# Kernel optimization log

Measured on AMD Instinct MI355X. Metric: run time of the kernel, lower is better.

The kernel has to match this reference:

```python
import jax, jax.numpy as jnp
import numpy as np

NUM_HEADS = 8
NEG_INF = float(-2**32 + 1)
LN_EPS = 1e-8


def setup_inputs() -> dict:
    key = jax.random.key(0)
    ks = jax.random.split(key, 9)
    B, T, D = 4, 2048, 512
    inp = {
        "queries": jax.random.normal(ks[0], (B, T, D), jnp.float32),
        "keys": jax.random.normal(ks[1], (B, T, D), jnp.float32),
        "values": jax.random.normal(ks[2], (B, T, D), jnp.float32),
        "Wq": jax.random.normal(ks[3], (D, D), jnp.float32) / np.sqrt(D),
        "bq": jnp.zeros((D,), jnp.float32),
        "Wk": jax.random.normal(ks[4], (D, D), jnp.float32) / np.sqrt(D),
        "bk": jnp.zeros((D,), jnp.float32),
        "Wv": jax.random.normal(ks[5], (D, D), jnp.float32) / np.sqrt(D),
        "bv": jnp.zeros((D,), jnp.float32),
        "gamma": jnp.ones((D,), jnp.float32),
        "beta": jnp.zeros((D,), jnp.float32),
    }
    return inp


def _split_heads(x, h):
    # torch.cat(torch.chunk(x, h, dim=2), dim=0): [B,T,D] -> [h*B, T, D/h], head-major
    B, T, D = x.shape
    return x.reshape(B, T, h, D // h).transpose(2, 0, 1, 3).reshape(h * B, T, D // h)


def _merge_heads(x, h, B):
    # inverse: [h*B, T, dh] -> [B, T, h*dh]
    hB, T, dh = x.shape
    return x.reshape(h, B, T, dh).transpose(1, 2, 0, 3).reshape(B, T, h * dh)


def reference(queries, keys, values, Wq, bq, Wk, bk, Wv, bv, gamma, beta):
    h = NUM_HEADS
    B, Tq, D = queries.shape
    dh = D // h

    Q = jax.nn.relu(queries @ Wq + bq)
    K = jax.nn.relu(keys @ Wk + bk)
    V = jax.nn.relu(values @ Wv + bv)

    Q_ = _split_heads(Q, h)  # [h*B, Tq, dh]
    K_ = _split_heads(K, h)
    V_ = _split_heads(V, h)

    scores = jnp.einsum('bqd,bkd->bqk', Q_, K_) / jnp.sqrt(jnp.float32(dh))  # [h*B, Tq, Tk]

    # key padding mask: zero rows in `keys` get -inf scores
    key_mask = jnp.sign(jnp.abs(jnp.sum(keys, axis=-1)))  # [B, Tk]
    key_mask = jnp.tile(key_mask, (h, 1))  # [h*B, Tk]
    scores = jnp.where(key_mask[:, None, :] == 0.0, NEG_INF, scores)

    attn = jax.nn.softmax(scores, axis=-1)

    # query mask applied multiplicatively post-softmax
    query_mask = jnp.sign(jnp.abs(jnp.sum(queries, axis=-1)))  # [B, Tq]
    query_mask = jnp.tile(query_mask, (h, 1))  # [h*B, Tq]
    attn = attn * query_mask[:, :, None]

    out = jnp.einsum('bqk,bkd->bqd', attn, V_)  # [h*B, Tq, dh]
    out = _merge_heads(out, h, B) + queries  # residual

    # custom LayerNorm: torch.std is unbiased (ddof=1), eps added to std
    mean = out.mean(-1, keepdims=True)
    std = jnp.sqrt(out.var(-1, ddof=1, keepdims=True))
    return gamma * (out - mean) / (std + LN_EPS) + beta
```

## Files before the change

### kernel.cpp

```cpp
#include <hip/hip_runtime.h>


typedef __attribute__((ext_vector_type(8))) __bf16 bf16x8;
typedef __attribute__((ext_vector_type(4))) float f32x4;

#if __has_builtin(__builtin_amdgcn_exp2f)
#define EXP2F __builtin_amdgcn_exp2f
#else
#define EXP2F exp2f
#endif

#define QSCALE (0.125f * 1.4426950408889634f)

__device__ __forceinline__ unsigned short f2bf(float f) {
  return __builtin_bit_cast(unsigned short, (__bf16)f);
}
__device__ __forceinline__ unsigned pk2(float a, float b) {
  return (unsigned)f2bf(a) | ((unsigned)f2bf(b) << 16);
}
__device__ __forceinline__ f32x4 mfma16(bf16x8 a, bf16x8 b, f32x4 c) {
  return __builtin_amdgcn_mfma_f32_16x16x32_bf16(a, b, c, 0, 0, 0);
}
__device__ __forceinline__ bf16x8 ld_bf8(const unsigned short* p) {
  return *(const bf16x8*)p;
}
__device__ __forceinline__ void g2l16(const void* g, void* l) {
  __builtin_amdgcn_global_load_lds(
      (const __attribute__((address_space(1))) void*)g,
      (__attribute__((address_space(3))) void*)l, 16, 0, 0);
}

__global__ __launch_bounds__(256) void wt_kernel(const float* __restrict__ Wq,
                                                 const float* __restrict__ Wk,
                                                 const float* __restrict__ Wv,
                                                 unsigned short* __restrict__ Wt) {
  int idx = blockIdx.x * 256 + threadIdx.x;
  int o = idx * 8;
  int z = o >> 18;
  int rem = o & 262143;
  int n = rem >> 9;
  int k0 = rem & 511;
  const float* W = (z == 0) ? Wq : ((z == 1) ? Wk : Wv);
  unsigned int w[4];
#pragma unroll
  for (int i = 0; i < 4; ++i) {
    unsigned short lo = f2bf(W[(k0 + 2 * i) * 512 + n]);
    unsigned short hi = f2bf(W[(k0 + 2 * i + 1) * 512 + n]);
    w[i] = (unsigned)lo | ((unsigned)hi << 16);
  }
  *(uint4*)(Wt + o) = make_uint4(w[0], w[1], w[2], w[3]);
}

__global__ __launch_bounds__(256) void mask_kernel(const float* __restrict__ q,
                                                   const float* __restrict__ k,
                                                   float* __restrict__ qmask,
                                                   float* __restrict__ kmask) {
  int w = blockIdx.x * 4 + (threadIdx.x >> 6);
  int lane = threadIdx.x & 63;
  const float* src = (w < 8192) ? q : k;
  int row = w & 8191;
  const float4* p = (const float4*)(src + row * 512);
  float4 v1 = p[lane];
  float4 v2 = p[64 + lane];
  float s = v1.x + v1.y + v1.z + v1.w + v2.x + v2.y + v2.z + v2.w;
#pragma unroll
  for (int off = 32; off > 0; off >>= 1) s += __shfl_xor(s, off);
  if (lane == 0) {
    float m = (s == 0.0f) ? 0.0f : 1.0f;
    if (w < 8192) qmask[row] = m; else kmask[row] = m;
  }
}

__global__ __launch_bounds__(256, 3) void proj_kernel(
    const float* __restrict__ Xq, const float* __restrict__ Xk,
    const float* __restrict__ Xv, const float* __restrict__ bq,
    const float* __restrict__ bk, const float* __restrict__ bv,
    const unsigned short* __restrict__ Wt, unsigned short* __restrict__ Qb,
    unsigned short* __restrict__ Kb, unsigned short* __restrict__ Vt) {
  __shared__ float Asm[2][128][16];
  __shared__ unsigned short Bsm[128][32];

  int tid = threadIdx.x;
  int m0g = blockIdx.x * 128;
  int z = m0g >> 13;
  int m0 = m0g & 8191;
  int n0 = blockIdx.y * 128;
  const float* X = (z == 0) ? Xq : ((z == 1) ? Xk : Xv);
  const float* bias = (z == 0) ? bq : ((z == 1) ? bk : bv);
  const unsigned short* Wz = Wt + z * 262144;

  int w = tid >> 6, lane = tid & 63;
  int wm = w >> 1, wn = w & 1;
  int mrow = lane & 15, quad = lane >> 4;

  int srow = tid >> 2, schk = tid & 3;
  const float* gA = X + (m0 + srow) * 512 + schk * 4;
  const unsigned short* gB = Wz + (n0 + srow) * 512 + schk * 8;
  char* lA = (char*)&Asm[0][0][0] + tid * 16;
  char* lB = (char*)&Bsm[0][0] + tid * 16;

  const float* rA = &Asm[quad >> 1][0][(quad & 1) * 8];
  const unsigned short* rB = &Bsm[0][quad * 8];

  f32x4 zero = {0.f, 0.f, 0.f, 0.f};
  f32x4 acc[4][4];
#pragma unroll
  for (int i = 0; i < 4; ++i)
#pragma unroll
    for (int j = 0; j < 4; ++j) acc[i][j] = zero;

  for (int kc = 0; kc < 16; ++kc) {
    int ko = kc * 32;
    g2l16(gA + ko, lA);
    g2l16(gA + ko + 64 * 512, lA + 4096);
    g2l16(gA + ko + 16, lA + 8192);
    g2l16(gA + ko + 16 + 64 * 512, lA + 12288);
    g2l16(gB + ko, lB);
    g2l16(gB + ko + 64 * 512, lB + 4096);
    __syncthreads();

    bf16x8 af[4], bfr[4];
#pragma unroll
    for (int mt = 0; mt < 4; ++mt) {
      const float* pa = rA + (wm * 64 + mt * 16 + mrow) * 16;
      f32x4 lo = *(const f32x4*)pa;
      f32x4 hi = *(const f32x4*)(pa + 4);
      bf16x8 t;
      t[0] = (__bf16)lo[0]; t[1] = (__bf16)lo[1];
      t[2] = (__bf16)lo[2]; t[3] = (__bf16)lo[3];
      t[4] = (__bf16)hi[0]; t[5] = (__bf16)hi[1];
      t[6] = (__bf16)hi[2]; t[7] = (__bf16)hi[3];
      af[mt] = t;
    }
#pragma unroll
    for (int nt = 0; nt < 4; ++nt)
      bfr[nt] = ld_bf8(rB + (wn * 64 + nt * 16 + mrow) * 32);
#pragma unroll
    for (int mt = 0; mt < 4; ++mt)
#pragma unroll
      for (int nt = 0; nt < 4; ++nt)
        acc[mt][nt] = mfma16(af[mt], bfr[nt], acc[mt][nt]);
    __syncthreads();
  }

  if (z < 2) {
    unsigned short* dst = (z == 0) ? Qb : Kb;
    float sc = (z == 0) ? QSCALE : 1.0f;
#pragma unroll
    for (int nt = 0; nt < 4; ++nt) {
      int n = n0 + wn * 64 + nt * 16 + mrow;
      float bv_ = bias[n];
#pragma unroll
      for (int mt = 0; mt < 4; ++mt) {
        int m = m0 + wm * 64 + mt * 16 + quad * 4;
#pragma unroll
        for (int r = 0; r < 4; ++r) {
          float v = fmaxf(acc[mt][nt][r] + bv_, 0.f) * sc;
          dst[(m + r) * 512 + n] = f2bf(v);
        }
      }
    }
  } else {
#pragma unroll
    for (int nt = 0; nt < 4; ++nt) {
      int n = n0 + wn * 64 + nt * 16 + mrow;
      int hh = n >> 6, jj = n & 63;
      float bv_ = bias[n];
#pragma unroll
      for (int mt = 0; mt < 4; ++mt) {
        int grow = m0 + wm * 64 + mt * 16 + quad * 4;
        int bb = grow >> 11, tl = grow & 2047;
        float p0 = fmaxf(acc[mt][nt][0] + bv_, 0.f);
        float p1 = fmaxf(acc[mt][nt][1] + bv_, 0.f);
        float p2 = fmaxf(acc[mt][nt][2] + bv_, 0.f);
        float p3 = fmaxf(acc[mt][nt][3] + bv_, 0.f);
        *(uint2*)(Vt + ((hh * 4 + bb) * 64 + jj) * 2048 + tl) =
            make_uint2(pk2(p0, p1), pk2(p2, p3));
      }
    }
  }
}

__global__ __launch_bounds__(256) void attn_kernel(
    const unsigned short* __restrict__ Qb, const unsigned short* __restrict__ Kb,
    const unsigned short* __restrict__ Vt, const float* __restrict__ qmask,
    const float* __restrict__ kmask, const float* __restrict__ queries,
    float* __restrict__ out) {
  __shared__ unsigned short plds[4][64 * 40];
  __shared__ float lbuf[4][64];
  float* Obuf = (float*)&plds[0][0];

  int hb = blockIdx.x;
  int qt = blockIdx.y;
  int h = hb >> 2, b = hb & 3;
  int q0 = qt * 64;
  int tid = threadIdx.x;
  int w = tid >> 6, lane = tid & 63;
  int mrow = lane & 15, quad = lane >> 4;
  unsigned short* pw = &plds[w][0];

  bf16x8 qf[4][2];
  {
    const unsigned short* qp = Qb + (b * 2048 + q0 + mrow) * 512 + h * 64 + quad * 8;
#pragma unroll
    for (int qn = 0; qn < 4; ++qn) {
      qf[qn][0] = ld_bf8(qp + qn * 8192);
      qf[qn][1] = ld_bf8(qp + qn * 8192 + 32);
    }
  }

  f32x4 zero = {0.f, 0.f, 0.f, 0.f};
  f32x4 oacc[4][4];
#pragma unroll
  for (int i = 0; i < 4; ++i)
#pragma unroll
    for (int j = 0; j < 4; ++j) oacc[i][j] = zero;
  float lpart[4] = {0.f, 0.f, 0.f, 0.f};

  const int kidx = (b * 2048 + w * 32 + mrow) * 512 + h * 64 + quad * 8;
  const int vidx = (hb * 64 + mrow) * 2048 + w * 32 + quad * 8;
  const int kmi = b * 2048 + w * 32 + quad * 4;
  const int pbase = mrow * 40 + quad * 4;
  const int prd = mrow * 40 + quad * 8;

  bf16x8 kf[2][2];
#pragma unroll
  for (int mt = 0; mt < 2; ++mt) {
    kf[mt][0] = ld_bf8(Kb + kidx + mt * 8192);
    kf[mt][1] = ld_bf8(Kb + kidx + mt * 8192 + 32);
  }

  for (int it = 0; it < 16; ++it) {
    int kb = it << 7;
    f32x4 sacc[2][4];
#pragma unroll
    for (int mt = 0; mt < 2; ++mt)
#pragma unroll
      for (int qn = 0; qn < 4; ++qn) {
        f32x4 s = mfma16(kf[mt][0], qf[qn][0], zero);
        sacc[mt][qn] = mfma16(kf[mt][1], qf[qn][1], s);
      }
    bf16x8 vf[4];
#pragma unroll
    for (int dt = 0; dt < 4; ++dt) vf[dt] = ld_bf8(Vt + vidx + dt * 32768 + kb);
    f32x4 km[2];
    km[0] = *(const f32x4*)(kmask + kmi + kb);
    km[1] = *(const f32x4*)(kmask + kmi + kb + 16);
#pragma unroll
    for (int mt = 0; mt < 2; ++mt)
#pragma unroll
      for (int qn = 0; qn < 4; ++qn) {
        f32x4 p;
#pragma unroll
        for (int r = 0; r < 4; ++r) p[r] = EXP2F(sacc[mt][qn][r]) * km[mt][r];
        lpart[qn] += p[0] + p[1] + p[2] + p[3];
        *(uint2*)(pw + qn * 640 + pbase + mt * 16) =
            make_uint2(pk2(p[0], p[1]), pk2(p[2], p[3]));
      }
    bf16x8 pf[4];
#pragma unroll
    for (int qn = 0; qn < 4; ++qn) pf[qn] = ld_bf8(pw + qn * 640 + prd);
    int nkb = ((it + 1) & 15) << 7;
    bf16x8 nkf[2][2];
#pragma unroll
    for (int mt = 0; mt < 2; ++mt) {
      nkf[mt][0] = ld_bf8(Kb + kidx + nkb * 512 + mt * 8192);
      nkf[mt][1] = ld_bf8(Kb + kidx + nkb * 512 + mt * 8192 + 32);
    }
#pragma unroll
    for (int dt = 0; dt < 4; ++dt)
#pragma unroll
      for (int qn = 0; qn < 4; ++qn)
        oacc[dt][qn] = mfma16(vf[dt], pf[qn], oacc[dt][qn]);
#pragma unroll
    for (int mt = 0; mt < 2; ++mt) {
      kf[mt][0] = nkf[mt][0];
      kf[mt][1] = nkf[mt][1];
    }
  }

#pragma unroll
  for (int qn = 0; qn < 4; ++qn) {
    lpart[qn] += __shfl_xor(lpart[qn], 16);
    lpart[qn] += __shfl_xor(lpart[qn], 32);
  }
  if (quad == 0) {
#pragma unroll
    for (int qn = 0; qn < 4; ++qn) lbuf[w][qn * 16 + mrow] = lpart[qn];
  }
  __syncthreads();

  for (int ph = 0; ph < 4; ++ph) {
    if (w == ph) {
#pragma unroll
      for (int dt = 0; dt < 4; ++dt)
#pragma unroll
        for (int qn = 0; qn < 4; ++qn) {
          float* dst = Obuf + (qn * 16 + mrow) * 68 + dt * 16 + quad * 4;
          f32x4 v = oacc[dt][qn];
          if (ph) {
            v[0] += dst[0]; v[1] += dst[1]; v[2] += dst[2]; v[3] += dst[3];
          }
          dst[0] = v[0]; dst[1] = v[1]; dst[2] = v[2]; dst[3] = v[3];
        }
    }
    __syncthreads();
  }

#pragma unroll
  for (int i = 0; i < 4; ++i) {
    int qr = w * 16 + i * 4 + quad;
    float l = lbuf[0][qr] + lbuf[1][qr] + lbuf[2][qr] + lbuf[3][qr];
    int qg = b * 2048 + q0 + qr;
    float inv = qmask[qg] / l;
    const float* ob = Obuf + qr * 68 + mrow * 4;
    const float4 res = *(const float4*)(queries + qg * 512 + h * 64 + mrow * 4);
    float4 r;
    r.x = ob[0] * inv + res.x;
    r.y = ob[1] * inv + res.y;
    r.z = ob[2] * inv + res.z;
    r.w = ob[3] * inv + res.w;
    *(float4*)(out + qg * 512 + h * 64 + mrow * 4) = r;
  }
}

__global__ __launch_bounds__(256) void ln_kernel(float* __restrict__ out,
                                                 const float* __restrict__ gamma,
                                                 const float* __restrict__ beta) {
  int row = blockIdx.x * 4 + (threadIdx.x >> 6);
  int lane = threadIdx.x & 63;
  float* p = out + row * 512;
  float4 v1 = ((const float4*)p)[lane];
  float4 v2 = ((const float4*)p)[64 + lane];
  float s = v1.x + v1.y + v1.z + v1.w + v2.x + v2.y + v2.z + v2.w;
  float sq = v1.x * v1.x + v1.y * v1.y + v1.z * v1.z + v1.w * v1.w +
             v2.x * v2.x + v2.y * v2.y + v2.z * v2.z + v2.w * v2.w;
#pragma unroll
  for (int off = 32; off > 0; off >>= 1) {
    s += __shfl_xor(s, off);
    sq += __shfl_xor(sq, off);
  }
  float mean = s * (1.f / 512.f);
  float var = fmaxf((sq - 512.f * mean * mean) * (1.f / 511.f), 0.f);
  float inv = 1.f / (sqrtf(var) + 1e-8f);
  float4 g1 = ((const float4*)gamma)[lane];
  float4 g2 = ((const float4*)gamma)[64 + lane];
  float4 b1 = ((const float4*)beta)[lane];
  float4 b2 = ((const float4*)beta)[64 + lane];
  v1.x = g1.x * (v1.x - mean) * inv + b1.x;
  v1.y = g1.y * (v1.y - mean) * inv + b1.y;
  v1.z = g1.z * (v1.z - mean) * inv + b1.z;
  v1.w = g1.w * (v1.w - mean) * inv + b1.w;
  v2.x = g2.x * (v2.x - mean) * inv + b2.x;
  v2.y = g2.y * (v2.y - mean) * inv + b2.y;
  v2.z = g2.z * (v2.z - mean) * inv + b2.z;
  v2.w = g2.w * (v2.w - mean) * inv + b2.w;
  ((float4*)p)[lane] = v1;
  ((float4*)p)[64 + lane] = v2;
}

extern "C" void kernel_launch(void* const* d_in, const int* in_sizes, int n_in,
                              void* d_out, int out_size, void* d_ws, size_t ws_size,
                              hipStream_t stream) {
  (void)in_sizes; (void)n_in; (void)out_size; (void)ws_size;
  const float* queries = (const float*)d_in[0];
  const float* keys    = (const float*)d_in[1];
  const float* values  = (const float*)d_in[2];
  const float* Wq = (const float*)d_in[3];
  const float* bq = (const float*)d_in[4];
  const float* Wk = (const float*)d_in[5];
  const float* bk = (const float*)d_in[6];
  const float* Wv = (const float*)d_in[7];
  const float* bv = (const float*)d_in[8];
  const float* gamma = (const float*)d_in[9];
  const float* beta  = (const float*)d_in[10];
  float* out = (float*)d_out;

  char* ws = (char*)d_ws;
  unsigned short* Qb = (unsigned short*)(ws);
  unsigned short* Kb = (unsigned short*)(ws + 8 * 1024 * 1024);
  unsigned short* Vt = (unsigned short*)(ws + 16 * 1024 * 1024);
  unsigned short* Wt = (unsigned short*)(ws + 24 * 1024 * 1024);
  float* qmask = (float*)(ws + 24 * 1024 * 1024 + 3 * 512 * 512 * 2);
  float* kmask = qmask + 8192;

  wt_kernel<<<384, 256, 0, stream>>>(Wq, Wk, Wv, Wt);
  mask_kernel<<<4096, 256, 0, stream>>>(queries, keys, qmask, kmask);
  proj_kernel<<<dim3(192, 4), 256, 0, stream>>>(queries, keys, values, bq, bk, bv,
                                                Wt, Qb, Kb, Vt);
  attn_kernel<<<dim3(32, 32), 256, 0, stream>>>(Qb, Kb, Vt, qmask, kmask, queries, out);
  ln_kernel<<<2048, 256, 0, stream>>>(out, gamma, beta);
}
```

Before: 215.7 us.

## Feed softmax probabilities directly from registers into PV MFMA, drop LDS staging

Removes the per-wave LDS round-trip that converted the score accumulator layout into the B-operand layout for the P·V MFMA. Instead, the V operand is loaded with a permuted k-index (two 4-element chunks) so the probabilities packed straight from the S accumulators line up with it. The row-sum is now computed with an extra MFMA against a vector of ones instead of scalar adds and cross-lane shuffles. This cuts LDS traffic and shuffles but adds MFMA work and splits each V fragment into two narrower global loads.

```diff
diff --git a/kernel.cpp b/kernel.cpp
--- a/kernel.cpp
+++ b/kernel.cpp
@@ -186,9 +186,8 @@
     const unsigned short* __restrict__ Vt, const float* __restrict__ qmask,
     const float* __restrict__ kmask, const float* __restrict__ queries,
     float* __restrict__ out) {
-  __shared__ unsigned short plds[4][64 * 40];
+  __shared__ float Obuf[64 * 68];
   __shared__ float lbuf[4][64];
-  float* Obuf = (float*)&plds[0][0];
 
   int hb = blockIdx.x;
   int qt = blockIdx.y;
@@ -197,7 +196,6 @@
   int tid = threadIdx.x;
   int w = tid >> 6, lane = tid & 63;
   int mrow = lane & 15, quad = lane >> 4;
-  unsigned short* pw = &plds[w][0];
 
   bf16x8 qf[4][2];
   {
@@ -215,19 +213,23 @@
   for (int i = 0; i < 4; ++i)
 #pragma unroll
     for (int j = 0; j < 4; ++j) oacc[i][j] = zero;
-  float lpart[4] = {0.f, 0.f, 0.f, 0.f};
-
-  const int kidx = (b * 2048 + w * 32 + mrow) * 512 + h * 64 + quad * 8;
-  const int vidx = (hb * 64 + mrow) * 2048 + w * 32 + quad * 8;
-  const int kmi = b * 2048 + w * 32 + quad * 4;
-  const int pbase = mrow * 40 + quad * 4;
-  const int prd = mrow * 40 + quad * 8;
+  f32x4 lacc[4];
+#pragma unroll
+  for (int i = 0; i < 4; ++i) lacc[i] = zero;
+
+  bf16x8 ones;
+#pragma unroll
+  for (int i = 0; i < 8; ++i) ones[i] = (__bf16)1.0f;
+
+  const unsigned short* kpB = Kb + (b * 2048 + w * 32 + mrow) * 512 + h * 64 + quad * 8;
+  const unsigned short* vpB = Vt + (hb * 64 + mrow) * 2048 + w * 32 + quad * 4;
+  const float* kmB = kmask + b * 2048 + w * 32 + quad * 4;
 
   bf16x8 kf[2][2];
 #pragma unroll
   for (int mt = 0; mt < 2; ++mt) {
-    kf[mt][0] = ld_bf8(Kb + kidx + mt * 8192);
-    kf[mt][1] = ld_bf8(Kb + kidx + mt * 8192 + 32);
+    kf[mt][0] = ld_bf8(kpB + mt * 8192);
+    kf[mt][1] = ld_bf8(kpB + mt * 8192 + 32);
   }
 
   for (int it = 0; it < 16; ++it) {
@@ -240,38 +242,39 @@
         f32x4 s = mfma16(kf[mt][0], qf[qn][0], zero);
         sacc[mt][qn] = mfma16(kf[mt][1], qf[qn][1], s);
       }
-    bf16x8 vf[4];
-#pragma unroll
-    for (int dt = 0; dt < 4; ++dt) vf[dt] = ld_bf8(Vt + vidx + dt * 32768 + kb);
-    f32x4 km[2];
-    km[0] = *(const f32x4*)(kmask + kmi + kb);
-    km[1] = *(const f32x4*)(kmask + kmi + kb + 16);
-#pragma unroll
-    for (int mt = 0; mt < 2; ++mt)
-#pragma unroll
-      for (int qn = 0; qn < 4; ++qn) {
-        f32x4 p;
-#pragma unroll
-        for (int r = 0; r < 4; ++r) p[r] = EXP2F(sacc[mt][qn][r]) * km[mt][r];
-        lpart[qn] += p[0] + p[1] + p[2] + p[3];
-        *(uint2*)(pw + qn * 640 + pbase + mt * 16) =
-            make_uint2(pk2(p[0], p[1]), pk2(p[2], p[3]));
-      }
-    bf16x8 pf[4];
-#pragma unroll
-    for (int qn = 0; qn < 4; ++qn) pf[qn] = ld_bf8(pw + qn * 640 + prd);
     int nkb = ((it + 1) & 15) << 7;
     bf16x8 nkf[2][2];
 #pragma unroll
     for (int mt = 0; mt < 2; ++mt) {
-      nkf[mt][0] = ld_bf8(Kb + kidx + nkb * 512 + mt * 8192);
-      nkf[mt][1] = ld_bf8(Kb + kidx + nkb * 512 + mt * 8192 + 32);
-    }
-#pragma unroll
-    for (int dt = 0; dt < 4; ++dt)
-#pragma unroll
-      for (int qn = 0; qn < 4; ++qn)
-        oacc[dt][qn] = mfma16(vf[dt], pf[qn], oacc[dt][qn]);
+      nkf[mt][0] = ld_bf8(kpB + nkb * 512 + mt * 8192);
+      nkf[mt][1] = ld_bf8(kpB + nkb * 512 + mt * 8192 + 32);
+    }
+    bf16x8 vf[4];
+#pragma unroll
+    for (int dt = 0; dt < 4; ++dt) {
+      const unsigned short* vp = vpB + dt * 32768 + kb;
+      uint2 lo = *(const uint2*)vp;
+      uint2 hi = *(const uint2*)(vp + 16);
+      vf[dt] = __builtin_bit_cast(bf16x8, make_uint4(lo.x, lo.y, hi.x, hi.y));
+    }
+    f32x4 km0 = *(const f32x4*)(kmB + kb);
+    f32x4 km1 = *(const f32x4*)(kmB + kb + 16);
+#pragma unroll
+    for (int qn = 0; qn < 4; ++qn) {
+      f32x4 p0, p1;
+#pragma unroll
+      for (int r = 0; r < 4; ++r) {
+        p0[r] = EXP2F(sacc[0][qn][r]) * km0[r];
+        p1[r] = EXP2F(sacc[1][qn][r]) * km1[r];
+      }
+      bf16x8 pf = __builtin_bit_cast(
+          bf16x8, make_uint4(pk2(p0[0], p0[1]), pk2(p0[2], p0[3]),
+                             pk2(p1[0], p1[1]), pk2(p1[2], p1[3])));
+      lacc[qn] = mfma16(ones, pf, lacc[qn]);
+#pragma unroll
+      for (int dt = 0; dt < 4; ++dt)
+        oacc[dt][qn] = mfma16(vf[dt], pf, oacc[dt][qn]);
+    }
 #pragma unroll
     for (int mt = 0; mt < 2; ++mt) {
       kf[mt][0] = nkf[mt][0];
@@ -279,14 +282,9 @@
     }
   }
 
-#pragma unroll
-  for (int qn = 0; qn < 4; ++qn) {
-    lpart[qn] += __shfl_xor(lpart[qn], 16);
-    lpart[qn] += __shfl_xor(lpart[qn], 32);
-  }
   if (quad == 0) {
 #pragma unroll
-    for (int qn = 0; qn < 4; ++qn) lbuf[w][qn * 16 + mrow] = lpart[qn];
+    for (int qn = 0; qn < 4; ++qn) lbuf[w][qn * 16 + mrow] = lacc[qn][0];
   }
   __syncthreads();
 
```

Measured after the change: 238.7 us. 1.11x slower.
